# Optimization experiments

Hardware: AMD Instinct MI355X
Metric: run time of the kernel (lower is better)

Reference implementation:

```python
import jax, jax.numpy as jnp
import numpy as np

N_QUBITS = 9
N_LAYERS = 2
N_ACTIONS = 1
K = 3  # kernel size
DIM = 1 << N_QUBITS  # 512 state-vector length


def _apply_1q(state, mat, q):
    """Apply a 2x2 gate on wire q (wire 0 = most significant bit, PennyLane convention).
    state: (N, DIM) complex64. mat: (2,2) shared or (N,2,2) per-sample."""
    a = 1 << q
    b = 1 << (N_QUBITS - 1 - q)
    s = state.reshape(-1, a, 2, b)
    if mat.ndim == 2:
        out = jnp.einsum('ij,najb->naib', mat, s)
    else:
        out = jnp.einsum('nij,najb->naib', mat, s)
    return out.reshape(state.shape)


def _cnot_perm(c, t):
    """Index permutation implementing CNOT(control=c, target=t) on the 512-dim basis."""
    idx = np.arange(DIM)
    cbit = (idx >> (N_QUBITS - 1 - c)) & 1
    return np.where(cbit == 1, idx ^ (1 << (N_QUBITS - 1 - t)), idx)


def _circuit(inputs, weights):
    """Batched state-vector simulation of: AngleEmbedding(RX) + StronglyEntanglingLayers.
    inputs: (N, 9) float. weights: (n_layers, 9, 3) float. Returns (N, N_ACTIONS) expval PauliZ."""
    N = inputs.shape[0]
    state = jnp.zeros((N, DIM), jnp.complex64).at[:, 0].set(1.0)

    # AngleEmbedding: RX(x_q) on each wire (per-sample angles)
    half = inputs.astype(jnp.float32) * 0.5
    c = jnp.cos(half).astype(jnp.complex64)
    s = (-1j * jnp.sin(half)).astype(jnp.complex64)
    for q in range(N_QUBITS):
        row0 = jnp.stack([c[:, q], s[:, q]], axis=-1)
        row1 = jnp.stack([s[:, q], c[:, q]], axis=-1)
        mat = jnp.stack([row0, row1], axis=-2)  # (N,2,2)
        state = _apply_1q(state, mat, q)

    # StronglyEntanglingLayers: per layer, Rot on each wire then CNOT ring of range r
    for l in range(N_LAYERS):
        phi, theta, omega = weights[l, :, 0], weights[l, :, 1], weights[l, :, 2]
        ct = jnp.cos(theta * 0.5).astype(jnp.complex64)
        st = jnp.sin(theta * 0.5).astype(jnp.complex64)
        ep = jnp.exp(-0.5j * (phi + omega).astype(jnp.complex64))  # e^{-i(phi+omega)/2}
        em = jnp.exp(0.5j * (phi - omega).astype(jnp.complex64))   # e^{+i(phi-omega)/2}
        for q in range(N_QUBITS):
            # Rot(phi,theta,omega) = RZ(omega) RY(theta) RZ(phi)
            mat = jnp.stack([
                jnp.stack([ep[q] * ct[q], -em[q] * st[q]]),
                jnp.stack([jnp.conj(em[q]) * st[q], jnp.conj(ep[q]) * ct[q]]),
            ]).astype(jnp.complex64)
            state = _apply_1q(state, mat, q)
        r = (l % (N_QUBITS - 1)) + 1  # PennyLane default ranges
        for q in range(N_QUBITS):
            state = state[:, _cnot_perm(q, (q + r) % N_QUBITS)]

    probs = state.real ** 2 + state.imag ** 2  # (N, DIM)
    idx = np.arange(DIM)
    exps = []
    for w in range(N_ACTIONS):
        z = (1.0 - 2.0 * ((idx >> (N_QUBITS - 1 - w)) & 1)).astype(np.float32)
        exps.append(probs @ jnp.asarray(z))
    return jnp.stack(exps, axis=-1)  # (N, N_ACTIONS)


def setup_inputs() -> dict:
    key = jax.random.key(0)
    k1, k2 = jax.random.split(key)
    x = jax.random.normal(k1, (8, 1, 64, 64), dtype=jnp.float32)
    # TorchLayer default init: uniform in [0, 2*pi)
    weights = jax.random.uniform(k2, (N_LAYERS, N_QUBITS, 3), dtype=jnp.float32) * (2.0 * np.pi)
    return {"x": x, "weights": weights}


def reference(x, weights):
    b, ch, h, w = x.shape
    # unfold(kernel=3, padding=1): patch feature k = ki*3+kj taken at (i+ki-1, j+kj-1)
    xp = jnp.pad(x, ((0, 0), (0, 0), (1, 1), (1, 1)))
    patches = jnp.stack(
        [xp[:, 0, ki:ki + h, kj:kj + w] for ki in range(K) for kj in range(K)],
        axis=-1,
    )  # (B, H, W, 9) -- matches unfold().transpose(1,2).reshape(-1,9) row order
    inputs = patches.reshape(-1, K * K)
    q_out = _circuit(inputs, weights)          # (B*H*W, n_actions)
    return q_out.reshape(b, h, w, -1).transpose(0, 3, 1, 2)  # (B, n_actions, H, W)
```

## Files before the change

kernel.cpp:

```cpp
#include <hip/hip_runtime.h>


#if defined(__clang__)
#pragma float_control(precise, off)
#endif

struct C2 { float r, i; };
__device__ __forceinline__ C2 cmul(C2 a, C2 b) {
    return C2{a.r * b.r - a.i * b.i, a.r * b.i + a.i * b.r};
}
__device__ __forceinline__ C2 cadd(C2 a, C2 b) { return C2{a.r + b.r, a.i + b.i}; }

__global__ __launch_bounds__(64) void qsim_kernel(const float* __restrict__ x,
                                                  const float* __restrict__ w,
                                                  float* __restrict__ out,
                                                  int nsamples) {
    __shared__ float rm[9][8];
    __shared__ float hm[5][3];
    const int tid = threadIdx.x;
    if (tid < 9) {
        const int q = tid;
        const float phi = w[q * 3 + 0], theta = w[q * 3 + 1], omega = w[q * 3 + 2];
        float st, ct, sp, cp, sm, cm;
        __sincosf(0.5f * theta, &st, &ct);
        __sincosf(0.5f * (phi + omega), &sp, &cp);
        __sincosf(0.5f * (phi - omega), &sm, &cm);
        float* m = rm[q];
        m[0] =  cp * ct; m[1] = -sp * ct;
        m[2] = -cm * st; m[3] = -sm * st;
        m[4] =  cm * st; m[5] = -sm * st;
        m[6] =  cp * ct; m[7] =  sp * ct;
    } else if (tid >= 16 && tid < 21) {
        const int i = tid - 16;
        const int qs[5] = {0, 1, 3, 5, 7};
        const int q = qs[i];
        const float phi = w[27 + q * 3 + 0], theta = w[27 + q * 3 + 1];
        float stt, ctt, sf, cf;
        __sincosf(theta, &stt, &ctt);
        __sincosf(phi, &sf, &cf);
        hm[i][0] = ctt;
        hm[i][1] = -stt * cf;
        hm[i][2] = -stt * sf;
    }
    __syncthreads();

    const int n = (blockIdx.x << 6) + tid;
    if (n >= nsamples) return;
    const int b  = n >> 12;
    const int i0 = (n >> 6) & 63;
    const int j0 = n & 63;

    float br0[9], bi0[9], br1[9], bi1[9];
    #pragma unroll
    for (int ki = 0; ki < 3; ++ki) {
        #pragma unroll
        for (int kj = 0; kj < 3; ++kj) {
            const int q = ki * 3 + kj;
            const int ii = i0 + ki - 1, jj = j0 + kj - 1;
            float a = 0.0f;
            if (ii >= 0 && ii < 64 && jj >= 0 && jj < 64)
                a = x[(b << 12) + (ii << 6) + jj];
            float s, c;
            __sincosf(0.5f * a, &s, &c);
            const float* m = rm[q];
            br0[q] = m[0] * c + m[3] * s;
            bi0[q] = m[1] * c - m[2] * s;
            br1[q] = m[4] * c + m[7] * s;
            bi1[q] = m[5] * c - m[6] * s;
        }
    }

    float Zb[9], Xb[9], Yb[9];
    #pragma unroll
    for (int m = 0; m < 9; ++m) {
        const int q = 8 - m;
        Zb[m] = (br0[q] * br0[q] + bi0[q] * bi0[q]) - (br1[q] * br1[q] + bi1[q] * bi1[q]);
        Xb[m] = 2.0f * (br0[q] * br1[q] + bi0[q] * bi1[q]);
        Yb[m] = 2.0f * (br0[q] * bi1[q] - bi0[q] * br1[q]);
    }

    C2 F[9][2][2];
    #pragma unroll
    for (int m = 0; m < 9; ++m) {
        F[m][0][0] = C2{1.0f, 0.0f};
        F[m][1][0] = C2{Zb[m], 0.0f};
        F[m][0][1] = C2{Xb[m], 0.0f};
        F[m][1][1] = C2{0.0f, Yb[m]};
    }

    C2 K[5][3];
    #pragma unroll
    for (int i = 0; i < 5; ++i) {
        K[i][0] = C2{hm[i][0], 0.0f};
        K[i][1] = C2{hm[i][1], 0.0f};
        K[i][2] = C2{0.0f, hm[i][2]};
    }

    const int A[3] = {1, 0, 1};
    const int B[3] = {0, 1, 1};

    C2 S7[2][3];
    #pragma unroll
    for (int t5 = 0; t5 < 2; ++t5) {
        #pragma unroll
        for (int c8 = 0; c8 < 3; ++c8) {
            const int a8 = A[c8], b8 = B[c8];
            C2 acc = C2{0.0f, 0.0f};
            #pragma unroll
            for (int c7 = 0; c7 < 3; ++c7) {
                const int a7 = A[c7], b7 = B[c7];
                C2 v = cmul(K[1][c7], F[6][t5][b7]);
                v = cmul(v, F[7][t5 ^ a7][b7 ^ b8]);
                v = cmul(v, F[8][t5 ^ a8 ^ a7][b8]);
                acc = cadd(acc, v);
            }
            S7[t5][c8] = acc;
        }
    }

    C2 S5[2][3];
    #pragma unroll
    for (int t3 = 0; t3 < 2; ++t3) {
        #pragma unroll
        for (int c8 = 0; c8 < 3; ++c8) {
            C2 acc = C2{0.0f, 0.0f};
            #pragma unroll
            for (int c5 = 0; c5 < 3; ++c5) {
                const int a5 = A[c5], b5 = B[c5];
                C2 v = cmul(K[2][c5], F[4][t3][b5]);
                v = cmul(v, F[5][t3 ^ a5][b5]);
                v = cmul(v, S7[t3 ^ a5][c8]);
                acc = cadd(acc, v);
            }
            S5[t3][c8] = acc;
        }
    }

    C2 S3[2][3];
    #pragma unroll
    for (int t1 = 0; t1 < 2; ++t1) {
        #pragma unroll
        for (int c8 = 0; c8 < 3; ++c8) {
            C2 acc = C2{0.0f, 0.0f};
            #pragma unroll
            for (int c3 = 0; c3 < 3; ++c3) {
                const int a3 = A[c3], b3 = B[c3];
                C2 v = cmul(K[3][c3], F[2][t1][b3]);
                v = cmul(v, F[3][t1 ^ a3][b3]);
                v = cmul(v, S5[t1 ^ a3][c8]);
                acc = cadd(acc, v);
            }
            S3[t1][c8] = acc;
        }
    }

    C2 S1[3];
    #pragma unroll
    for (int c8 = 0; c8 < 3; ++c8) {
        const int a8 = A[c8];
        C2 acc = C2{0.0f, 0.0f};
        #pragma unroll
        for (int c1 = 0; c1 < 3; ++c1) {
            const int a1 = A[c1], b1 = B[c1];
            C2 v = cmul(K[4][c1], F[0][a8][b1]);
            v = cmul(v, F[1][a8 ^ a1][b1]);
            v = cmul(v, S3[a8 ^ a1][c8]);
            acc = cadd(acc, v);
        }
        S1[c8] = acc;
    }

    float E = 0.0f;
    #pragma unroll
    for (int c8 = 0; c8 < 3; ++c8)
        E += K[0][c8].r * S1[c8].r - K[0][c8].i * S1[c8].i;

    out[n] = E;
}

extern "C" void kernel_launch(void* const* d_in, const int* in_sizes, int n_in,
                              void* d_out, int out_size, void* d_ws, size_t ws_size,
                              hipStream_t stream) {
    const float* x = (const float*)d_in[0];
    const float* w = (const float*)d_in[1];
    float* out = (float*)d_out;
    const int nsamples = out_size;
    const int blocks = (nsamples + 63) >> 6;
    qsim_kernel<<<blocks, 64, 0, stream>>>(x, w, out, nsamples);
}
```

Measured before the change: 9.843 us.

## Split tensor contraction across two waves per sample and precompute Bloch coefficients

```diff
diff --git a/kernel.cpp b/kernel.cpp
--- a/kernel.cpp
+++ b/kernel.cpp
@@ -11,12 +11,106 @@
 }
 __device__ __forceinline__ C2 cadd(C2 a, C2 b) { return C2{a.r + b.r, a.i + b.i}; }
 
-__global__ __launch_bounds__(64) void qsim_kernel(const float* __restrict__ x,
-                                                  const float* __restrict__ w,
-                                                  float* __restrict__ out,
-                                                  int nsamples) {
-    __shared__ float rm[9][8];
+template<int C8BASE, int NC8>
+__device__ __forceinline__ float dp_eval(const float (&Zb)[9], const float (&Xb)[9],
+                                         const float (&Yb)[9], const float (&hm)[5][3]) {
+    C2 F[9][2][2];
+    #pragma unroll
+    for (int m = 0; m < 9; ++m) {
+        F[m][0][0] = C2{1.0f, 0.0f};
+        F[m][1][0] = C2{Zb[m], 0.0f};
+        F[m][0][1] = C2{Xb[m], 0.0f};
+        F[m][1][1] = C2{0.0f, Yb[m]};
+    }
+    C2 K[5][3];
+    #pragma unroll
+    for (int i = 0; i < 5; ++i) {
+        K[i][0] = C2{hm[i][0], 0.0f};
+        K[i][1] = C2{hm[i][1], 0.0f};
+        K[i][2] = C2{0.0f, hm[i][2]};
+    }
+    const int A[3] = {1, 0, 1};
+    const int B[3] = {0, 1, 1};
+
+    C2 S7[2][NC8];
+    #pragma unroll
+    for (int t5 = 0; t5 < 2; ++t5) {
+        #pragma unroll
+        for (int c8i = 0; c8i < NC8; ++c8i) {
+            const int c8 = C8BASE + c8i;
+            const int a8 = A[c8], b8 = B[c8];
+            C2 acc = C2{0.0f, 0.0f};
+            #pragma unroll
+            for (int c7 = 0; c7 < 3; ++c7) {
+                const int a7 = A[c7], b7 = B[c7];
+                C2 v = cmul(K[1][c7], F[6][t5][b7]);
+                v = cmul(v, F[7][t5 ^ a7][b7 ^ b8]);
+                v = cmul(v, F[8][t5 ^ a8 ^ a7][b8]);
+                acc = cadd(acc, v);
+            }
+            S7[t5][c8i] = acc;
+        }
+    }
+    C2 S5[2][NC8];
+    #pragma unroll
+    for (int t3 = 0; t3 < 2; ++t3) {
+        #pragma unroll
+        for (int c8i = 0; c8i < NC8; ++c8i) {
+            C2 acc = C2{0.0f, 0.0f};
+            #pragma unroll
+            for (int c5 = 0; c5 < 3; ++c5) {
+                const int a5 = A[c5], b5 = B[c5];
+                C2 v = cmul(K[2][c5], F[4][t3][b5]);
+                v = cmul(v, F[5][t3 ^ a5][b5]);
+                v = cmul(v, S7[t3 ^ a5][c8i]);
+                acc = cadd(acc, v);
+            }
+            S5[t3][c8i] = acc;
+        }
+    }
+    C2 S3[2][NC8];
+    #pragma unroll
+    for (int t1 = 0; t1 < 2; ++t1) {
+        #pragma unroll
+        for (int c8i = 0; c8i < NC8; ++c8i) {
+            C2 acc = C2{0.0f, 0.0f};
+            #pragma unroll
+            for (int c3 = 0; c3 < 3; ++c3) {
+                const int a3 = A[c3], b3 = B[c3];
+                C2 v = cmul(K[3][c3], F[2][t1][b3]);
+                v = cmul(v, F[3][t1 ^ a3][b3]);
+                v = cmul(v, S5[t1 ^ a3][c8i]);
+                acc = cadd(acc, v);
+            }
+            S3[t1][c8i] = acc;
+        }
+    }
+    float E = 0.0f;
+    #pragma unroll
+    for (int c8i = 0; c8i < NC8; ++c8i) {
+        const int c8 = C8BASE + c8i;
+        const int a8 = A[c8];
+        C2 acc = C2{0.0f, 0.0f};
+        #pragma unroll
+        for (int c1 = 0; c1 < 3; ++c1) {
+            const int a1 = A[c1], b1 = B[c1];
+            C2 v = cmul(K[4][c1], F[0][a8][b1]);
+            v = cmul(v, F[1][a8 ^ a1][b1]);
+            v = cmul(v, S3[a8 ^ a1][c8i]);
+            acc = cadd(acc, v);
+        }
+        E += K[0][c8].r * acc.r - K[0][c8].i * acc.i;
+    }
+    return E;
+}
+
+__global__ __launch_bounds__(128) void qsim_kernel(const float* __restrict__ x,
+                                                   const float* __restrict__ w,
+                                                   float* __restrict__ out,
+                                                   int nsamples) {
+    __shared__ float cb[9][6];
     __shared__ float hm[5][3];
+    __shared__ float part[64];
     const int tid = threadIdx.x;
     if (tid < 9) {
         const int q = tid;
@@ -25,11 +119,18 @@
         __sincosf(0.5f * theta, &st, &ct);
         __sincosf(0.5f * (phi + omega), &sp, &cp);
         __sincosf(0.5f * (phi - omega), &sm, &cm);
-        float* m = rm[q];
-        m[0] =  cp * ct; m[1] = -sp * ct;
-        m[2] = -cm * st; m[3] = -sm * st;
-        m[4] =  cm * st; m[5] = -sm * st;
-        m[6] =  cp * ct; m[7] =  sp * ct;
+        const float m00r =  cp * ct, m00i = -sp * ct;
+        const float m01r = -cm * st, m01i = -sm * st;
+        const float m10r =  cm * st, m10i = -sm * st;
+        const float m11r =  cp * ct, m11i =  sp * ct;
+        cb[q][0] = (m00r * m00r + m00i * m00i) - (m10r * m10r + m10i * m10i);
+        cb[q][2] = 2.0f * (m00r * m10r + m00i * m10i);
+        cb[q][4] = 2.0f * (m00r * m10i - m00i * m10r);
+        const float u0r = m00r - m01i, u0i = m00i + m01r;
+        const float u1r = m10r - m11i, u1i = m10i + m11r;
+        cb[q][1] = 0.5f * ((u0r * u0r + u0i * u0i) - (u1r * u1r + u1i * u1i));
+        cb[q][3] = (u0r * u1r + u0i * u1i);
+        cb[q][5] = (u0r * u1i - u0i * u1r);
     } else if (tid >= 16 && tid < 21) {
         const int i = tid - 16;
         const int qs[5] = {0, 1, 3, 5, 7};
@@ -44,138 +145,40 @@
     }
     __syncthreads();
 
-    const int n = (blockIdx.x << 6) + tid;
-    if (n >= nsamples) return;
-    const int b  = n >> 12;
-    const int i0 = (n >> 6) & 63;
-    const int j0 = n & 63;
-
-    float br0[9], bi0[9], br1[9], bi1[9];
-    #pragma unroll
-    for (int ki = 0; ki < 3; ++ki) {
-        #pragma unroll
-        for (int kj = 0; kj < 3; ++kj) {
-            const int q = ki * 3 + kj;
-            const int ii = i0 + ki - 1, jj = j0 + kj - 1;
-            float a = 0.0f;
-            if (ii >= 0 && ii < 64 && jj >= 0 && jj < 64)
-                a = x[(b << 12) + (ii << 6) + jj];
-            float s, c;
-            __sincosf(0.5f * a, &s, &c);
-            const float* m = rm[q];
-            br0[q] = m[0] * c + m[3] * s;
-            bi0[q] = m[1] * c - m[2] * s;
-            br1[q] = m[4] * c + m[7] * s;
-            bi1[q] = m[5] * c - m[6] * s;
-        }
-    }
-
-    float Zb[9], Xb[9], Yb[9];
-    #pragma unroll
-    for (int m = 0; m < 9; ++m) {
-        const int q = 8 - m;
-        Zb[m] = (br0[q] * br0[q] + bi0[q] * bi0[q]) - (br1[q] * br1[q] + bi1[q] * bi1[q]);
-        Xb[m] = 2.0f * (br0[q] * br1[q] + bi0[q] * bi1[q]);
-        Yb[m] = 2.0f * (br0[q] * bi1[q] - bi0[q] * br1[q]);
-    }
-
-    C2 F[9][2][2];
-    #pragma unroll
-    for (int m = 0; m < 9; ++m) {
-        F[m][0][0] = C2{1.0f, 0.0f};
-        F[m][1][0] = C2{Zb[m], 0.0f};
-        F[m][0][1] = C2{Xb[m], 0.0f};
-        F[m][1][1] = C2{0.0f, Yb[m]};
-    }
-
-    C2 K[5][3];
-    #pragma unroll
-    for (int i = 0; i < 5; ++i) {
-        K[i][0] = C2{hm[i][0], 0.0f};
-        K[i][1] = C2{hm[i][1], 0.0f};
-        K[i][2] = C2{0.0f, hm[i][2]};
-    }
-
-    const int A[3] = {1, 0, 1};
-    const int B[3] = {0, 1, 1};
-
-    C2 S7[2][3];
-    #pragma unroll
-    for (int t5 = 0; t5 < 2; ++t5) {
-        #pragma unroll
-        for (int c8 = 0; c8 < 3; ++c8) {
-            const int a8 = A[c8], b8 = B[c8];
-            C2 acc = C2{0.0f, 0.0f};
-            #pragma unroll
-            for (int c7 = 0; c7 < 3; ++c7) {
-                const int a7 = A[c7], b7 = B[c7];
-                C2 v = cmul(K[1][c7], F[6][t5][b7]);
-                v = cmul(v, F[7][t5 ^ a7][b7 ^ b8]);
-                v = cmul(v, F[8][t5 ^ a8 ^ a7][b8]);
-                acc = cadd(acc, v);
-            }
-            S7[t5][c8] = acc;
-        }
-    }
-
-    C2 S5[2][3];
-    #pragma unroll
-    for (int t3 = 0; t3 < 2; ++t3) {
-        #pragma unroll
-        for (int c8 = 0; c8 < 3; ++c8) {
-            C2 acc = C2{0.0f, 0.0f};
-            #pragma unroll
-            for (int c5 = 0; c5 < 3; ++c5) {
-                const int a5 = A[c5], b5 = B[c5];
-                C2 v = cmul(K[2][c5], F[4][t3][b5]);
-                v = cmul(v, F[5][t3 ^ a5][b5]);
-                v = cmul(v, S7[t3 ^ a5][c8]);
-                acc = cadd(acc, v);
-            }
-            S5[t3][c8] = acc;
-        }
-    }
-
-    C2 S3[2][3];
-    #pragma unroll
-    for (int t1 = 0; t1 < 2; ++t1) {
-        #pragma unroll
-        for (int c8 = 0; c8 < 3; ++c8) {
-            C2 acc = C2{0.0f, 0.0f};
-            #pragma unroll
-            for (int c3 = 0; c3 < 3; ++c3) {
-                const int a3 = A[c3], b3 = B[c3];
-                C2 v = cmul(K[3][c3], F[2][t1][b3]);
-                v = cmul(v, F[3][t1 ^ a3][b3]);
-                v = cmul(v, S5[t1 ^ a3][c8]);
-                acc = cadd(acc, v);
-            }
-            S3[t1][c8] = acc;
-        }
-    }
-
-    C2 S1[3];
-    #pragma unroll
-    for (int c8 = 0; c8 < 3; ++c8) {
-        const int a8 = A[c8];
-        C2 acc = C2{0.0f, 0.0f};
-        #pragma unroll
-        for (int c1 = 0; c1 < 3; ++c1) {
-            const int a1 = A[c1], b1 = B[c1];
-            C2 v = cmul(K[4][c1], F[0][a8][b1]);
-            v = cmul(v, F[1][a8 ^ a1][b1]);
-            v = cmul(v, S3[a8 ^ a1][c8]);
-            acc = cadd(acc, v);
-        }
-        S1[c8] = acc;
-    }
+    const int lane = tid & 63;
+    const int half = tid >> 6;
+    const int n = (blockIdx.x << 6) + lane;
 
     float E = 0.0f;
-    #pragma unroll
-    for (int c8 = 0; c8 < 3; ++c8)
-        E += K[0][c8].r * S1[c8].r - K[0][c8].i * S1[c8].i;
+    if (n < nsamples) {
+        const int b  = n >> 12;
+        const int i0 = (n >> 6) & 63;
+        const int j0 = n & 63;
 
-    out[n] = E;
+        float Zb[9], Xb[9], Yb[9];
+        #pragma unroll
+        for (int ki = 0; ki < 3; ++ki) {
+            #pragma unroll
+            for (int kj = 0; kj < 3; ++kj) {
+                const int q = ki * 3 + kj;
+                const int m = 8 - q;
+                const int ii = i0 + ki - 1, jj = j0 + kj - 1;
+                float a = 0.0f;
+                if (ii >= 0 && ii < 64 && jj >= 0 && jj < 64)
+                    a = x[(b << 12) + (ii << 6) + jj];
+                float sa, ca;
+                __sincosf(a, &sa, &ca);
+                Zb[m] = ca * cb[q][0] - sa * cb[q][1];
+                Xb[m] = ca * cb[q][2] - sa * cb[q][3];
+                Yb[m] = ca * cb[q][4] - sa * cb[q][5];
+            }
+        }
+        if (half == 0) E = dp_eval<0, 1>(Zb, Xb, Yb, hm);
+        else           E = dp_eval<1, 2>(Zb, Xb, Yb, hm);
+    }
+    if (half) part[lane] = E;
+    __syncthreads();
+    if (!half && n < nsamples) out[n] = E + part[lane];
 }
 
 extern "C" void kernel_launch(void* const* d_in, const int* in_sizes, int n_in,
@@ -186,5 +189,5 @@
     float* out = (float*)d_out;
     const int nsamples = out_size;
     const int blocks = (nsamples + 63) >> 6;
-    qsim_kernel<<<blocks, 64, 0, stream>>>(x, w, out, nsamples);
+    qsim_kernel<<<blocks, 128, 0, stream>>>(x, w, out, nsamples);
 }
```

Result: faster. 9.403 us (-4.5%).
